# Optimization experiments

Measured on AMD Instinct MI355X. Metric: run time of the kernel, lower is better.

Reference implementation:

```python
import jax, jax.numpy as jnp
import numpy as np

N_NODES = 50000
N_EDGES = 1_600_000
F_IN = 128
HIDDEN = 128
N_REL = 8
N_GRAPHS = 64


def setup_inputs() -> dict:
    key = jax.random.key(0)
    ks = jax.random.split(key, 16)
    x = jax.random.normal(ks[0], (N_NODES, F_IN), dtype=jnp.float32)
    edge_index = jax.random.randint(ks[1], (2, N_EDGES), 0, N_NODES, dtype=jnp.int32)
    edge_type = jax.random.randint(ks[2], (N_EDGES,), 0, N_REL, dtype=jnp.int32)
    edge_attr = jax.nn.one_hot(edge_type, N_REL, dtype=jnp.float32)  # one-hot relation encoding
    batch = jnp.sort(jax.random.randint(ks[3], (N_NODES,), 0, N_GRAPHS, dtype=jnp.int32))
    s = 1.0 / np.sqrt(F_IN)
    params = {}
    dims = [(F_IN, HIDDEN), (HIDDEN, HIDDEN), (HIDDEN, HIDDEN)]
    for i, (fi, fo) in enumerate(dims, 1):
        params[f"W{i}"] = jax.random.normal(ks[3 + 3 * i], (N_REL, fi, fo), dtype=jnp.float32) * s
        params[f"root{i}"] = jax.random.normal(ks[4 + 3 * i], (fi, fo), dtype=jnp.float32) * s
        params[f"b{i}"] = jnp.zeros((fo,), dtype=jnp.float32)
    lin_w = jax.random.normal(ks[13], (HIDDEN, HIDDEN), dtype=jnp.float32) * (1.0 / np.sqrt(HIDDEN))
    lin_b = jnp.zeros((HIDDEN,), dtype=jnp.float32)
    return {"x": x, "edge_index": edge_index, "edge_attr": edge_attr, "batch": batch,
            **params, "lin_w": lin_w, "lin_b": lin_b}


def _rgcn_conv(x, src, dst, edge_type, W, root, bias):
    # PyG RGCNConv with aggr='mean': per-relation mean of transformed neighbors + root + bias.
    # Mean is linear, so aggregate raw features per (dst, relation) then apply W_r.
    n = x.shape[0]
    seg = dst * N_REL + edge_type                      # combined segment id [E]
    msg = x[src]                                       # [E, F_in] gather
    agg = jax.ops.segment_sum(msg, seg, num_segments=n * N_REL)
    cnt = jax.ops.segment_sum(jnp.ones((src.shape[0],), x.dtype), seg, num_segments=n * N_REL)
    agg = agg / jnp.maximum(cnt, 1.0)[:, None]
    agg = agg.reshape(n, N_REL, -1)                    # [N, R, F_in]
    return jnp.einsum('nri,rio->no', agg, W) + x @ root + bias


def reference(x, edge_index, edge_attr, batch,
              W1, root1, b1, W2, root2, b2, W3, root3, b3, lin_w, lin_b):
    src, dst = edge_index[0], edge_index[1]
    edge_type = jnp.argmax(edge_attr, axis=1)          # np.where(edge_attr == 1)[1]
    h = jax.nn.relu(_rgcn_conv(x, src, dst, edge_type, W1, root1, b1))
    h = jax.nn.relu(_rgcn_conv(h, src, dst, edge_type, W2, root2, b2))
    h = jax.nn.relu(_rgcn_conv(h, src, dst, edge_type, W3, root3, b3))
    # global_mean_pool over graphs
    sums = jax.ops.segment_sum(h, batch, num_segments=N_GRAPHS)
    cnts = jax.ops.segment_sum(jnp.ones((h.shape[0],), h.dtype), batch, num_segments=N_GRAPHS)
    pooled = sums / jnp.maximum(cnts, 1.0)[:, None]    # [G, hidden]
    return pooled @ lin_w + lin_b
```

## Files before the change

kernel.cpp:

```cpp
#include <hip/hip_runtime.h>
#include <hip/hip_fp16.h>

#define N_NODESC 50000
#define N_EDGESC 1600000
#define FEAT 128
#define NREL 8
#define NSEG (N_NODESC * NREL)
#define NGRAPH 64
#define KTOT 1152
#define NKC 36
#define WPACK_ELEMS (NKC * 4 * 128 * 8)
#define WPACK_BLKS (WPACK_ELEMS / 256)
#define NHALF (N_NODESC * FEAT)
#define CVT_BLKS ((NHALF / 4 + 255) / 256)

typedef float f32x4 __attribute__((ext_vector_type(4)));
typedef _Float16 f16x8 __attribute__((ext_vector_type(8)));

static inline size_t align256(size_t x) { return (x + 255) & ~(size_t)255; }

__device__ __forceinline__ float4 h4tof4(uint2 r) {
  const __half* h = (const __half*)&r;
  return make_float4(__half2float(h[0]), __half2float(h[1]),
                     __half2float(h[2]), __half2float(h[3]));
}

__global__ void k_zero(int* __restrict__ p, int n) {
  int i = blockIdx.x * blockDim.x + threadIdx.x;
  int stride = gridDim.x * blockDim.x;
  for (; i < n; i += stride) p[i] = 0;
}

__global__ void k_edge_hist(const int* __restrict__ ei, const float* __restrict__ eattr,
                            int* __restrict__ seg, int* __restrict__ cnt) {
  int e = blockIdx.x * blockDim.x + threadIdx.x;
  if (e >= N_EDGESC) return;
  int dst = ei[N_EDGESC + e];
  const float4* ap = (const float4*)(eattr + (size_t)e * 8);
  float4 a0 = ap[0], a1 = ap[1];
  int ty = 0;
  if (a0.y > 0.5f) ty = 1;
  if (a0.z > 0.5f) ty = 2;
  if (a0.w > 0.5f) ty = 3;
  if (a1.x > 0.5f) ty = 4;
  if (a1.y > 0.5f) ty = 5;
  if (a1.z > 0.5f) ty = 6;
  if (a1.w > 0.5f) ty = 7;
  int s = dst * NREL + ty;
  seg[e] = s;
  atomicAdd(&cnt[s], 1);
}

__global__ void k_scan1(const int* __restrict__ cnt, int* __restrict__ outIncl,
                        int* __restrict__ bsums, int n) {
  __shared__ int sd[256];
  int t = threadIdx.x;
  int base = blockIdx.x * 4096 + t * 16;
  int v[16];
  int s = 0;
#pragma unroll
  for (int j = 0; j < 16; ++j) {
    int idx = base + j;
    int x = (idx < n) ? cnt[idx] : 0;
    s += x;
    v[j] = s;
  }
  sd[t] = s;
  __syncthreads();
  for (int off = 1; off < 256; off <<= 1) {
    int add = (t >= off) ? sd[t - off] : 0;
    __syncthreads();
    sd[t] += add;
    __syncthreads();
  }
  int prev = (t > 0) ? sd[t - 1] : 0;
#pragma unroll
  for (int j = 0; j < 16; ++j) {
    int idx = base + j;
    if (idx < n) outIncl[idx] = prev + v[j];
  }
  if (t == 255) bsums[blockIdx.x] = sd[255];
}

__global__ void k_scan2(int* __restrict__ bsums, int nb) {
  __shared__ int sd[128];
  int t = threadIdx.x;
  int v = (t < nb) ? bsums[t] : 0;
  sd[t] = v;
  __syncthreads();
  for (int off = 1; off < 128; off <<= 1) {
    int add = (t >= off) ? sd[t - off] : 0;
    __syncthreads();
    sd[t] += add;
    __syncthreads();
  }
  if (t < nb) bsums[t] = sd[t] - v;
}

__global__ void k_scan3(int* __restrict__ offsets, const int* __restrict__ bsums, int n) {
  int i = blockIdx.x * blockDim.x + threadIdx.x;
  if (i == 0) offsets[0] = 0;
  if (i < n) offsets[i + 1] += bsums[i >> 12];
}

__global__ void k_scatter(const int* __restrict__ ei, const int* __restrict__ seg,
                          const int* __restrict__ offsets, int* __restrict__ cursor,
                          int* __restrict__ ssrc) {
  int e = blockIdx.x * blockDim.x + threadIdx.x;
  if (e >= N_EDGESC) return;
  int s = seg[e];
  int p = offsets[s] + atomicAdd(&cursor[s], 1);
  ssrc[p] = ei[e];
}

__global__ void k_prep(const float* __restrict__ W1, const float* __restrict__ r1,
                       const float* __restrict__ W2, const float* __restrict__ r2,
                       const float* __restrict__ W3, const float* __restrict__ r3,
                       const float* __restrict__ x,
                       __half* __restrict__ whi3, __half* __restrict__ wlo3,
                       __half* __restrict__ p0) {
  int b = blockIdx.x;
  if (b < 3 * WPACK_BLKS) {
    int L = b / WPACK_BLKS;
    int idx = (b - L * WPACK_BLKS) * 256 + threadIdx.x;
    const float* W = (L == 0) ? W1 : (L == 1) ? W2 : W3;
    const float* root = (L == 0) ? r1 : (L == 1) ? r2 : r3;
    int j = idx & 7;
    int n = (idx >> 3) & 127;
    int slot = idx >> 10;
    int k = slot * 8 + j;
    float v = (k < 1024) ? W[(size_t)k * 128 + n] : root[(size_t)(k - 1024) * 128 + n];
    __half hi = __float2half(v);
    float lof = v - __half2float(hi);
    whi3[(size_t)L * WPACK_ELEMS + idx] = hi;
    wlo3[(size_t)L * WPACK_ELEMS + idx] = __float2half(lof);
  } else {
    int i = (b - 3 * WPACK_BLKS) * 256 + threadIdx.x;
    if (i * 4 < NHALF) {
      float4 v = *(const float4*)&x[i * 4];
      __half h[4] = {__float2half(v.x), __float2half(v.y),
                     __float2half(v.z), __float2half(v.w)};
      *(uint2*)&p0[(size_t)i * 4] = *(uint2*)h;
    }
  }
}

__global__ __launch_bounds__(256, 8) void k_agg(
    const __half* __restrict__ in, const int* __restrict__ offsets,
    const int* __restrict__ ssrc, __half* __restrict__ agg,
    int nodeBase, int nodeCount) {
  int t = blockIdx.x * blockDim.x + threadIdx.x;
  int un = t >> 5;
  int l = t & 31;
  if (un >= nodeCount) return;
  int node = nodeBase + un;
  for (int r = 0; r < NREL; ++r) {
    int sidx = node * NREL + r;
    int beg = offsets[sidx], end = offsets[sidx + 1];
    float4 s = make_float4(0.f, 0.f, 0.f, 0.f);
    for (int base = beg; base < end; base += 4) {
      int last = end - 1;
      int e1 = base + 1 <= last ? base + 1 : last;
      int e2 = base + 2 <= last ? base + 2 : last;
      int e3 = base + 3 <= last ? base + 3 : last;
      int i0 = ssrc[base], i1 = ssrc[e1], i2 = ssrc[e2], i3 = ssrc[e3];
      uint2 r0 = *(const uint2*)&in[(size_t)i0 * FEAT + l * 4];
      uint2 r1 = *(const uint2*)&in[(size_t)i1 * FEAT + l * 4];
      uint2 r2 = *(const uint2*)&in[(size_t)i2 * FEAT + l * 4];
      uint2 r3 = *(const uint2*)&in[(size_t)i3 * FEAT + l * 4];
      float4 v0 = h4tof4(r0), v1 = h4tof4(r1), v2 = h4tof4(r2), v3 = h4tof4(r3);
      s.x += v0.x; s.y += v0.y; s.z += v0.z; s.w += v0.w;
      if (base + 1 < end) { s.x += v1.x; s.y += v1.y; s.z += v1.z; s.w += v1.w; }
      if (base + 2 < end) { s.x += v2.x; s.y += v2.y; s.z += v2.z; s.w += v2.w; }
      if (base + 3 < end) { s.x += v3.x; s.y += v3.y; s.z += v3.z; s.w += v3.w; }
    }
    int c = end - beg;
    if (c > 1) {
      float inv = 1.0f / (float)c;
      s.x *= inv; s.y *= inv; s.z *= inv; s.w *= inv;
    }
    __half hv[4] = {__float2half(s.x), __float2half(s.y), __float2half(s.z), __float2half(s.w)};
    *(uint2*)&agg[((size_t)un * NREL + r) * FEAT + l * 4] = *(uint2*)hv;
  }
}

__global__ __launch_bounds__(256, 4) void k_gemm_mfma(
    const __half* __restrict__ aggc,
    const __half* __restrict__ xin,
    const __half* __restrict__ Whi, const __half* __restrict__ Wlo,
    const float* __restrict__ bias, __half* __restrict__ out16,
    int n0g, int rows) {
  __shared__ __half Ah[2][2048] __attribute__((aligned(16)));
  __shared__ __half Bh[2][4096] __attribute__((aligned(16)));
  __shared__ __half Bl[2][4096] __attribute__((aligned(16)));

  const int t = threadIdx.x;
  const int lane = t & 63, wave = t >> 6;
  const int l15 = lane & 15, lg = lane >> 4;
  const int wrow0 = wave * 16;
  const int m0 = blockIdx.x * 64;
  const int srow = t >> 2, sseg = t & 3;

  int rowc = srow;
  if (m0 + rowc >= rows) rowc = rows - 1 - m0;
  if (rowc < 0) rowc = 0;
  const __half* aggRow = aggc + (size_t)(m0 + rowc) * 1024 + sseg * 8;
  const __half* xRow = xin + (size_t)(n0g + m0 + rowc) * FEAT + sseg * 8;

  uint4 av0, sbh0, sbh1, sbl0, sbl1;

#define LOADC(kc)                                                         \
  {                                                                       \
    const __half* asrc = ((kc) < 32) ? (aggRow + (kc) * 32)               \
                                     : (xRow + ((kc) - 32) * 32);         \
    av0 = *(const uint4*)asrc;                                            \
    const uint4* bhs = (const uint4*)(Whi + (size_t)(kc) * 4096);         \
    const uint4* bls = (const uint4*)(Wlo + (size_t)(kc) * 4096);         \
    sbh0 = bhs[t * 2]; sbh1 = bhs[t * 2 + 1];                             \
    sbl0 = bls[t * 2]; sbl1 = bls[t * 2 + 1];                             \
  }
#define WRITEC(b)                                                         \
  {                                                                       \
    *(uint4*)&Ah[b][(sseg * 64 + srow) * 8] = av0;                        \
    ((uint4*)Bh[b])[t * 2] = sbh0; ((uint4*)Bh[b])[t * 2 + 1] = sbh1;     \
    ((uint4*)Bl[b])[t * 2] = sbl0; ((uint4*)Bl[b])[t * 2 + 1] = sbl1;     \
  }

  f32x4 acc[8];
#pragma unroll
  for (int b = 0; b < 8; ++b) acc[b] = (f32x4){0.f, 0.f, 0.f, 0.f};

  LOADC(0);
  WRITEC(0);
  LOADC(1);
  __syncthreads();

  for (int kc = 0; kc < NKC; ++kc) {
    const int cur = kc & 1;
    f16x8 af = *(const f16x8*)&Ah[cur][(lg * 64 + wrow0 + l15) * 8];
#pragma unroll
    for (int nf = 0; nf < 8; ++nf) {
      int bn = nf * 16 + l15;
      f16x8 vh = *(const f16x8*)&Bh[cur][(lg * 128 + bn) * 8];
      f16x8 vl = *(const f16x8*)&Bl[cur][(lg * 128 + bn) * 8];
      acc[nf] = __builtin_amdgcn_mfma_f32_16x16x32_f16(af, vh, acc[nf], 0, 0, 0);
      acc[nf] = __builtin_amdgcn_mfma_f32_16x16x32_f16(af, vl, acc[nf], 0, 0, 0);
    }
    if (kc < NKC - 1) {
      WRITEC(cur ^ 1);
      if (kc < NKC - 2) LOADC(kc + 2);
      __syncthreads();
    }
  }
#undef LOADC
#undef WRITEC

  float bcol[8];
#pragma unroll
  for (int nf = 0; nf < 8; ++nf) bcol[nf] = bias[nf * 16 + l15];
#pragma unroll
  for (int nf = 0; nf < 8; ++nf)
#pragma unroll
    for (int j = 0; j < 4; ++j) {
      int grow = m0 + wrow0 + lg * 4 + j;
      if (grow < rows) {
        float v = acc[nf][j] + bcol[nf];
        v = v > 0.f ? v : 0.f;
        out16[(size_t)(n0g + grow) * FEAT + nf * 16 + l15] = __float2half(v);
      }
    }
}

__global__ void k_pool(const __half* __restrict__ h, const int* __restrict__ batch,
                       const float* __restrict__ lw, const float* __restrict__ lb,
                       float* __restrict__ out) {
  __shared__ float sums[8][128];
  __shared__ float prow[128];
  int gidx = blockIdx.x, t = threadIdx.x;
  int f = t & 127, grp = t >> 7;
  int lo = 0, hi = N_NODESC;
  while (lo < hi) {
    int mid = (lo + hi) >> 1;
    if (batch[mid] < gidx) lo = mid + 1; else hi = mid;
  }
  int start = lo;
  hi = N_NODESC;
  while (lo < hi) {
    int mid = (lo + hi) >> 1;
    if (batch[mid] < gidx + 1) lo = mid + 1; else hi = mid;
  }
  int end = lo;
  float s = 0.f;
  for (int n = start + grp; n < end; n += 8) s += __half2float(h[(size_t)n * FEAT + f]);
  sums[grp][f] = s;
  __syncthreads();
  if (grp == 0) {
    float tot = 0.f;
#pragma unroll
    for (int gg = 0; gg < 8; ++gg) tot += sums[gg][f];
    int c = end - start;
    prow[f] = (c > 0) ? tot / (float)c : 0.f;
  }
  __syncthreads();
  float a = 0.f;
  for (int k = grp * 16; k < grp * 16 + 16; ++k) a = fmaf(prow[k], lw[(size_t)k * FEAT + f], a);
  __syncthreads();
  sums[grp][f] = a;
  __syncthreads();
  if (grp == 0) {
    float tot = lb[f];
#pragma unroll
    for (int gg = 0; gg < 8; ++gg) tot += sums[gg][f];
    out[(size_t)gidx * FEAT + f] = tot;
  }
}

extern "C" void kernel_launch(void* const* d_in, const int* in_sizes, int n_in,
                              void* d_out, int out_size, void* d_ws, size_t ws_size,
                              hipStream_t stream) {
  const float* x = (const float*)d_in[0];
  const int* ei = (const int*)d_in[1];
  const float* eattr = (const float*)d_in[2];
  const int* batch = (const int*)d_in[3];
  const float* Wl[3] = {(const float*)d_in[4], (const float*)d_in[7], (const float*)d_in[10]};
  const float* rl[3] = {(const float*)d_in[5], (const float*)d_in[8], (const float*)d_in[11]};
  const float* bl[3] = {(const float*)d_in[6], (const float*)d_in[9], (const float*)d_in[12]};
  const float* lw = (const float*)d_in[13];
  const float* lb = (const float*)d_in[14];
  float* out = (float*)d_out;
  (void)n_in; (void)in_sizes; (void)out_size;

  size_t pos = 0;
  char* base = (char*)d_ws;
  auto alloc = [&](size_t bytes) { char* q = base + pos; pos += align256(bytes); return q; };
  int* seg = (int*)alloc(sizeof(int) * (size_t)N_EDGESC);
  int* cntcur = (int*)alloc(sizeof(int) * (size_t)2 * NSEG);
  int* cnt = cntcur;
  int* cursor = cntcur + NSEG;
  int* offsets = (int*)alloc(sizeof(int) * (size_t)(NSEG + 1));
  int* bsums = (int*)alloc(sizeof(int) * 1024);
  int* ssrc = (int*)alloc(sizeof(int) * (size_t)N_EDGESC);
  __half* p0 = (__half*)alloc(sizeof(__half) * (size_t)NHALF);
  __half* p1 = (__half*)alloc(sizeof(__half) * (size_t)NHALF);
  __half* whi3 = (__half*)alloc(sizeof(__half) * (size_t)3 * WPACK_ELEMS);
  __half* wlo3 = (__half*)alloc(sizeof(__half) * (size_t)3 * WPACK_ELEMS);
  size_t remain = (ws_size > pos) ? (ws_size - pos) : 0;
  long long cn = (long long)(remain / (sizeof(__half) * NREL * FEAT));
  int chunkNodes = (cn > N_NODESC) ? N_NODESC : (int)cn;
  chunkNodes &= ~127;
  if (chunkNodes < 128) chunkNodes = 128;
  __half* aggbuf = (__half*)(base + pos);
  int nchunks = (N_NODESC + chunkNodes - 1) / chunkNodes;

  hipLaunchKernelGGL(k_zero, dim3(2048), dim3(256), 0, stream, cntcur, 2 * NSEG);
  hipLaunchKernelGGL(k_edge_hist, dim3((N_EDGESC + 255) / 256), dim3(256), 0, stream,
                     ei, eattr, seg, cnt);
  int nbScan = (NSEG + 4095) / 4096;
  hipLaunchKernelGGL(k_scan1, dim3(nbScan), dim3(256), 0, stream, cnt, offsets + 1, bsums, NSEG);
  hipLaunchKernelGGL(k_scan2, dim3(1), dim3(128), 0, stream, bsums, nbScan);
  hipLaunchKernelGGL(k_scan3, dim3((NSEG + 255) / 256), dim3(256), 0, stream, offsets, bsums, NSEG);
  hipLaunchKernelGGL(k_scatter, dim3((N_EDGESC + 255) / 256), dim3(256), 0, stream,
                     ei, seg, offsets, cursor, ssrc);

  hipLaunchKernelGGL(k_prep, dim3(3 * WPACK_BLKS + CVT_BLKS), dim3(256), 0, stream,
                     Wl[0], rl[0], Wl[1], rl[1], Wl[2], rl[2], x, whi3, wlo3, p0);

  const __half* inPtr = p0;
  __half* outPtr = p1;
  for (int L = 0; L < 3; ++L) {
    const __half* whi = whi3 + (size_t)L * WPACK_ELEMS;
    const __half* wlo = wlo3 + (size_t)L * WPACK_ELEMS;
    for (int c = 0; c < nchunks; ++c) {
      int nodeBase = c * chunkNodes;
      int rowsC = N_NODESC - nodeBase;
      if (rowsC > chunkNodes) rowsC = chunkNodes;
      int aggBlocks = (rowsC * 32 + 255) / 256;
      hipLaunchKernelGGL(k_agg, dim3(aggBlocks), dim3(256), 0, stream,
                         inPtr, offsets, ssrc, aggbuf, nodeBase, rowsC);
      hipLaunchKernelGGL(k_gemm_mfma, dim3((rowsC + 63) / 64), dim3(256), 0, stream,
                         aggbuf, inPtr, whi, wlo, bl[L], outPtr, nodeBase, rowsC);
    }
    const __half* tmp = inPtr;
    inPtr = outPtr;
    outPtr = (__half*)tmp;
  }

  hipLaunchKernelGGL(k_pool, dim3(NGRAPH), dim3(1024), 0, stream, p1, batch, lw, lb, out);
}
```

Measured before the change: 753.7 us.

## Double GEMM row tile to 128 per block and use nontemporal agg traffic

The MFMA GEMM now handles 128 rows per block instead of 64. Each wave computes two 16-row fragments, so every weight fragment loaded from LDS is reused twice and the weight tile is fetched from global memory half as often per row. The aggregation buffer is written and read with nontemporal hints to keep it from displacing reusable data in cache. In exchange the kernel uses more LDS and registers per block, occupancy drops to 3 blocks per CU, and there are half as many blocks per chunk.

Result: no change. 755.7 us (+0.3%).

```diff
diff --git a/kernel.cpp b/kernel.cpp
--- a/kernel.cpp
+++ b/kernel.cpp
@@ -16,10 +16,12 @@
 
 typedef float f32x4 __attribute__((ext_vector_type(4)));
 typedef _Float16 f16x8 __attribute__((ext_vector_type(8)));
+typedef unsigned int u32x2 __attribute__((ext_vector_type(2)));
+typedef unsigned int u32x4 __attribute__((ext_vector_type(4)));
 
 static inline size_t align256(size_t x) { return (x + 255) & ~(size_t)255; }
 
-__device__ __forceinline__ float4 h4tof4(uint2 r) {
+__device__ __forceinline__ float4 h4tof4(u32x2 r) {
   const __half* h = (const __half*)&r;
   return make_float4(__half2float(h[0]), __half2float(h[1]),
                      __half2float(h[2]), __half2float(h[3]));
@@ -164,10 +166,10 @@
       int e2 = base + 2 <= last ? base + 2 : last;
       int e3 = base + 3 <= last ? base + 3 : last;
       int i0 = ssrc[base], i1 = ssrc[e1], i2 = ssrc[e2], i3 = ssrc[e3];
-      uint2 r0 = *(const uint2*)&in[(size_t)i0 * FEAT + l * 4];
-      uint2 r1 = *(const uint2*)&in[(size_t)i1 * FEAT + l * 4];
-      uint2 r2 = *(const uint2*)&in[(size_t)i2 * FEAT + l * 4];
-      uint2 r3 = *(const uint2*)&in[(size_t)i3 * FEAT + l * 4];
+      u32x2 r0 = *(const u32x2*)&in[(size_t)i0 * FEAT + l * 4];
+      u32x2 r1 = *(const u32x2*)&in[(size_t)i1 * FEAT + l * 4];
+      u32x2 r2 = *(const u32x2*)&in[(size_t)i2 * FEAT + l * 4];
+      u32x2 r3 = *(const u32x2*)&in[(size_t)i3 * FEAT + l * 4];
       float4 v0 = h4tof4(r0), v1 = h4tof4(r1), v2 = h4tof4(r2), v3 = h4tof4(r3);
       s.x += v0.x; s.y += v0.y; s.z += v0.z; s.w += v0.w;
       if (base + 1 < end) { s.x += v1.x; s.y += v1.y; s.z += v1.z; s.w += v1.w; }
@@ -180,55 +182,66 @@
       s.x *= inv; s.y *= inv; s.z *= inv; s.w *= inv;
     }
     __half hv[4] = {__float2half(s.x), __float2half(s.y), __float2half(s.z), __float2half(s.w)};
-    *(uint2*)&agg[((size_t)un * NREL + r) * FEAT + l * 4] = *(uint2*)hv;
-  }
-}
-
-__global__ __launch_bounds__(256, 4) void k_gemm_mfma(
+    __builtin_nontemporal_store(*(u32x2*)hv,
+                                (u32x2*)&agg[((size_t)un * NREL + r) * FEAT + l * 4]);
+  }
+}
+
+__global__ __launch_bounds__(256, 3) void k_gemm_mfma(
     const __half* __restrict__ aggc,
     const __half* __restrict__ xin,
     const __half* __restrict__ Whi, const __half* __restrict__ Wlo,
     const float* __restrict__ bias, __half* __restrict__ out16,
     int n0g, int rows) {
-  __shared__ __half Ah[2][2048] __attribute__((aligned(16)));
+  __shared__ __half Ah[2][4096] __attribute__((aligned(16)));
   __shared__ __half Bh[2][4096] __attribute__((aligned(16)));
   __shared__ __half Bl[2][4096] __attribute__((aligned(16)));
 
   const int t = threadIdx.x;
   const int lane = t & 63, wave = t >> 6;
   const int l15 = lane & 15, lg = lane >> 4;
-  const int wrow0 = wave * 16;
-  const int m0 = blockIdx.x * 64;
-  const int srow = t >> 2, sseg = t & 3;
+  const int wrow0 = wave * 32;
+  const int m0 = blockIdx.x * 128;
+  const int srow = t >> 1, half = t & 1;
 
   int rowc = srow;
   if (m0 + rowc >= rows) rowc = rows - 1 - m0;
   if (rowc < 0) rowc = 0;
-  const __half* aggRow = aggc + (size_t)(m0 + rowc) * 1024 + sseg * 8;
-  const __half* xRow = xin + (size_t)(n0g + m0 + rowc) * FEAT + sseg * 8;
-
-  uint4 av0, sbh0, sbh1, sbl0, sbl1;
-
-#define LOADC(kc)                                                         \
-  {                                                                       \
-    const __half* asrc = ((kc) < 32) ? (aggRow + (kc) * 32)               \
-                                     : (xRow + ((kc) - 32) * 32);         \
-    av0 = *(const uint4*)asrc;                                            \
-    const uint4* bhs = (const uint4*)(Whi + (size_t)(kc) * 4096);         \
-    const uint4* bls = (const uint4*)(Wlo + (size_t)(kc) * 4096);         \
-    sbh0 = bhs[t * 2]; sbh1 = bhs[t * 2 + 1];                             \
-    sbl0 = bls[t * 2]; sbl1 = bls[t * 2 + 1];                             \
-  }
-#define WRITEC(b)                                                         \
-  {                                                                       \
-    *(uint4*)&Ah[b][(sseg * 64 + srow) * 8] = av0;                        \
-    ((uint4*)Bh[b])[t * 2] = sbh0; ((uint4*)Bh[b])[t * 2 + 1] = sbh1;     \
-    ((uint4*)Bl[b])[t * 2] = sbl0; ((uint4*)Bl[b])[t * 2 + 1] = sbl1;     \
-  }
-
-  f32x4 acc[8];
-#pragma unroll
-  for (int b = 0; b < 8; ++b) acc[b] = (f32x4){0.f, 0.f, 0.f, 0.f};
+  const __half* aggRow = aggc + (size_t)(m0 + rowc) * 1024 + half * 16;
+  const __half* xRow = xin + (size_t)(n0g + m0 + rowc) * FEAT + half * 16;
+
+  u32x4 av0, av1, sbh0, sbh1, sbl0, sbl1;
+
+#define LOADC(kc)                                                          \
+  {                                                                        \
+    if ((kc) < 32) {                                                       \
+      const u32x4* asrc = (const u32x4*)(aggRow + (kc) * 32);              \
+      av0 = __builtin_nontemporal_load(asrc);           \
+      av1 = __builtin_nontemporal_load(asrc + 1);                          \
+    } else {                                                               \
+      const u32x4* asrc = (const u32x4*)(xRow + ((kc) - 32) * 32);         \
+      av0 = asrc[0];                                 \
+      av1 = asrc[1];                                                       \
+    }                                                                      \
+    const u32x4* bhs = (const u32x4*)(Whi + (size_t)(kc) * 4096);          \
+    const u32x4* bls = (const u32x4*)(Wlo + (size_t)(kc) * 4096);          \
+    sbh0 = bhs[t * 2]; sbh1 = bhs[t * 2 + 1];                              \
+    sbl0 = bls[t * 2]; sbl1 = bls[t * 2 + 1];                              \
+  }
+#define WRITEC(b)                                                          \
+  {                                                                        \
+    int g0 = half * 2;                                                     \
+    *(u32x4*)&Ah[b][(g0 * 128 + srow) * 8] = av0;                          \
+    *(u32x4*)&Ah[b][((g0 + 1) * 128 + srow) * 8] = av1;                    \
+    ((u32x4*)Bh[b])[t * 2] = sbh0; ((u32x4*)Bh[b])[t * 2 + 1] = sbh1;      \
+    ((u32x4*)Bl[b])[t * 2] = sbl0; ((u32x4*)Bl[b])[t * 2 + 1] = sbl1;      \
+  }
+
+  f32x4 acc[2][8];
+#pragma unroll
+  for (int a = 0; a < 2; ++a)
+#pragma unroll
+    for (int b = 0; b < 8; ++b) acc[a][b] = (f32x4){0.f, 0.f, 0.f, 0.f};
 
   LOADC(0);
   WRITEC(0);
@@ -237,14 +250,21 @@
 
   for (int kc = 0; kc < NKC; ++kc) {
     const int cur = kc & 1;
-    f16x8 af = *(const f16x8*)&Ah[cur][(lg * 64 + wrow0 + l15) * 8];
+    f16x8 af[2];
+#pragma unroll
+    for (int mf = 0; mf < 2; ++mf) {
+      int ar = wrow0 + mf * 16 + l15;
+      af[mf] = *(const f16x8*)&Ah[cur][(lg * 128 + ar) * 8];
+    }
 #pragma unroll
     for (int nf = 0; nf < 8; ++nf) {
       int bn = nf * 16 + l15;
       f16x8 vh = *(const f16x8*)&Bh[cur][(lg * 128 + bn) * 8];
       f16x8 vl = *(const f16x8*)&Bl[cur][(lg * 128 + bn) * 8];
-      acc[nf] = __builtin_amdgcn_mfma_f32_16x16x32_f16(af, vh, acc[nf], 0, 0, 0);
-      acc[nf] = __builtin_amdgcn_mfma_f32_16x16x32_f16(af, vl, acc[nf], 0, 0, 0);
+      acc[0][nf] = __builtin_amdgcn_mfma_f32_16x16x32_f16(af[0], vh, acc[0][nf], 0, 0, 0);
+      acc[0][nf] = __builtin_amdgcn_mfma_f32_16x16x32_f16(af[0], vl, acc[0][nf], 0, 0, 0);
+      acc[1][nf] = __builtin_amdgcn_mfma_f32_16x16x32_f16(af[1], vh, acc[1][nf], 0, 0, 0);
+      acc[1][nf] = __builtin_amdgcn_mfma_f32_16x16x32_f16(af[1], vl, acc[1][nf], 0, 0, 0);
     }
     if (kc < NKC - 1) {
       WRITEC(cur ^ 1);
@@ -259,16 +279,18 @@
 #pragma unroll
   for (int nf = 0; nf < 8; ++nf) bcol[nf] = bias[nf * 16 + l15];
 #pragma unroll
-  for (int nf = 0; nf < 8; ++nf)
-#pragma unroll
-    for (int j = 0; j < 4; ++j) {
-      int grow = m0 + wrow0 + lg * 4 + j;
-      if (grow < rows) {
-        float v = acc[nf][j] + bcol[nf];
-        v = v > 0.f ? v : 0.f;
-        out16[(size_t)(n0g + grow) * FEAT + nf * 16 + l15] = __float2half(v);
+  for (int mf = 0; mf < 2; ++mf)
+#pragma unroll
+    for (int nf = 0; nf < 8; ++nf)
+#pragma unroll
+      for (int j = 0; j < 4; ++j) {
+        int grow = m0 + wrow0 + mf * 16 + lg * 4 + j;
+        if (grow < rows) {
+          float v = acc[mf][nf][j] + bcol[nf];
+          v = v > 0.f ? v : 0.f;
+          out16[(size_t)(n0g + grow) * FEAT + nf * 16 + l15] = __float2half(v);
+        }
       }
-    }
 }
 
 __global__ void k_pool(const __half* __restrict__ h, const int* __restrict__ batch,
@@ -377,7 +399,7 @@
       int aggBlocks = (rowsC * 32 + 255) / 256;
       hipLaunchKernelGGL(k_agg, dim3(aggBlocks), dim3(256), 0, stream,
                          inPtr, offsets, ssrc, aggbuf, nodeBase, rowsC);
-      hipLaunchKernelGGL(k_gemm_mfma, dim3((rowsC + 63) / 64), dim3(256), 0, stream,
+      hipLaunchKernelGGL(k_gemm_mfma, dim3((rowsC + 127) / 128), dim3(256), 0, stream,
                          aggbuf, inPtr, whi, wlo, bl[L], outPtr, nodeBase, rowsC);
     }
     const __half* tmp = inPtr;
```
